# Kernel optimization log

Measured on AMD Instinct MI355X. Metric: run time of the kernel, lower is better.

Reference implementation:

```python
import jax, jax.numpy as jnp
import numpy as np
import math

H, Dh, S = 8, 64, 3          # heads, dim per head, samples factor
B, T, N, K = 2, 12, 512, 16  # batch, time, nodes, local-adj width
F = H * Dh                   # features = 512
SN = int(S * math.log2(N))   # Sampled_Nodes = 27
EPS = 1e-5


def setup_inputs() -> dict:
    key = jax.random.key(0)
    ks = jax.random.split(key, 22)
    sc = 1.0 / math.sqrt(F)
    W = lambda k: jax.random.normal(k, (F, F), jnp.float32) * sc
    bb = lambda k: jax.random.normal(k, (F,), jnp.float32) * 0.01
    return {
        "x": jax.random.normal(ks[0], (B, T, N, F), jnp.float32),
        "spa_eigvalue": jax.random.normal(ks[1], (F,), jnp.float32) * 0.1,
        "spa_eigvec": jax.random.normal(ks[2], (N, F), jnp.float32) * 0.1,
        "tem_eigvalue": jax.random.normal(ks[3], (F,), jnp.float32) * 0.1,
        "tem_eigvec": jax.random.normal(ks[4], (N, F), jnp.float32) * 0.1,
        "localadj": jax.random.randint(ks[5], (N, K), 0, N),
        "Wq": W(ks[6]), "bq": bb(ks[7]),
        "Wk": W(ks[8]), "bk": bb(ks[9]),
        "Wv": W(ks[10]), "bv": bb(ks[11]),
        "Wo": W(ks[12]), "bo": bb(ks[13]),
        "w_proj": jax.random.normal(ks[14], (K,), jnp.float32) / math.sqrt(K),
        "b_proj": jax.random.normal(ks[15], (), jnp.float32) * 0.01,
        "gamma": jnp.ones((F,), jnp.float32),
        "beta": jnp.zeros((F,), jnp.float32),
        "W1": W(ks[16]), "b1": bb(ks[17]),
        "W2": W(ks[18]), "b2": bb(ks[19]),
    }


def _lin(v, Wm, bv):  # torch nn.Linear: y = x @ W^T + b, W is [out, in]
    return jnp.einsum('...i,oi->...o', v, Wm) + bv


def _ln(v, g=None, b=None):  # LayerNorm over last dim, eps=1e-5
    mu = jnp.mean(v, -1, keepdims=True)
    var = jnp.var(v, -1, keepdims=True)
    y = (v - mu) * jax.lax.rsqrt(var + EPS)
    return y * g + b if g is not None else y


def reference(x, spa_eigvalue, spa_eigvec, tem_eigvalue, tem_eigvec, localadj,
              Wq, bq, Wk, bk, Wv, bv, Wo, bo, w_proj, b_proj,
              gamma, beta, W1, b1, W2, b2):
    # eigvec @ diag(eigval) == row-wise scaling
    x_ = x + (spa_eigvec * spa_eigvalue + tem_eigvec * tem_eigvalue)
    to_heads = lambda v: v.reshape(B, T, N, H, Dh).transpose(3, 0, 1, 2, 4)  # [H,B,T,N,Dh]
    Qh = to_heads(_lin(x_, Wq, bq))
    Kh = to_heads(_lin(x_, Wk, bk))
    Vh = to_heads(_lin(x_, Wv, bv))
    # local-adjacency K sampling: [H,B,T,N,K,Dh]
    Ks = Kh[:, :, :, localadj, :]
    qks = jnp.einsum('hbtnd,hbtnkd->hbtnk', Qh, Ks)
    # importance score per query node via learned projection over K neighbors
    M = jnp.einsum('hbtnk,k->hbtn', qks, w_proj) + b_proj
    _, m_top = jax.lax.top_k(M, SN)                              # [H,B,T,SN]
    Qr = jnp.take_along_axis(Qh, m_top[..., None], axis=3)       # [H,B,T,SN,Dh]
    scores = jnp.einsum('hbtsd,hbtnd->hbtsn', Qr, Kh) / math.sqrt(Dh)
    attn = jax.nn.softmax(scores, axis=-1)                       # [H,B,T,SN,N]
    cp = jnp.argmax(attn, axis=-2)                               # best sampled query per key node [H,B,T,N]
    val = jnp.einsum('hbtsn,hbtnd->hbtsd', attn, Vh)             # [H,B,T,SN,Dh]
    out = jnp.take_along_axis(val, cp[..., None], axis=3)        # [H,B,T,N,Dh]
    out = out.transpose(1, 2, 3, 0, 4).reshape(B, T, N, F)       # merge heads
    v = _ln(_lin(out, Wo, bo), gamma, beta)
    h = jax.nn.relu(_lin(v, W1, b1))
    h = _lin(h, W2, b2) + v
    return _ln(h)
```

## Files before the change

### kernel.cpp

```cpp
#include <hip/hip_runtime.h>
#include <math.h>

#define H_    8
#define DH    64
#define NN    512
#define KADJ  16
#define FF    512
#define BTOT  24
#define ROWS  12288
#define SN_   27
#define EPS_  1e-5f

typedef short short8 __attribute__((ext_vector_type(8)));
typedef float f32x4  __attribute__((ext_vector_type(4)));

__device__ __forceinline__ ushort f2bf(float x) {
    uint u = __float_as_uint(x);
    u += 0x7FFFu + ((u >> 16) & 1u);
    return (ushort)(u >> 16);
}
__device__ __forceinline__ float bf2f(ushort h) {
    return __uint_as_float(((uint)h) << 16);
}
__device__ __forceinline__ void pack_hilo(float4 a, float4 b, short8& hi, short8& lo) {
    float v[8] = {a.x, a.y, a.z, a.w, b.x, b.y, b.z, b.w};
    #pragma unroll
    for (int j = 0; j < 8; ++j) {
        ushort h = f2bf(v[j]);
        hi[j] = (short)h;
        lo[j] = (short)f2bf(v[j] - bf2f(h));
    }
}

__device__ __forceinline__ void gload_lds16(const ushort* g, ushort* l) {
    __builtin_amdgcn_global_load_lds(
        (const __attribute__((address_space(1))) unsigned int*)g,
        (__attribute__((address_space(3))) unsigned int*)l,
        16, 0, 0);
}

__global__ __launch_bounds__(256) void add_pos_bf16(
    const float* __restrict__ x,
    const float* __restrict__ spa_val, const float* __restrict__ spa_vec,
    const float* __restrict__ tem_val, const float* __restrict__ tem_vec,
    ushort* __restrict__ xh, ushort* __restrict__ xl)
{
    int i = blockIdx.x * 256 + threadIdx.x;
    int f4  = i & 127;
    int row = i >> 7;
    int n   = row & (NN - 1);

    float4 xv = reinterpret_cast<const float4*>(x)[i];
    float4 sv = reinterpret_cast<const float4*>(spa_vec)[n * 128 + f4];
    float4 tv = reinterpret_cast<const float4*>(tem_vec)[n * 128 + f4];
    float4 se = reinterpret_cast<const float4*>(spa_val)[f4];
    float4 te = reinterpret_cast<const float4*>(tem_val)[f4];
    float r0 = xv.x + sv.x * se.x + tv.x * te.x;
    float r1 = xv.y + sv.y * se.y + tv.y * te.y;
    float r2 = xv.z + sv.z * se.z + tv.z * te.z;
    float r3 = xv.w + sv.w * se.w + tv.w * te.w;
    ushort h0 = f2bf(r0), h1 = f2bf(r1), h2 = f2bf(r2), h3 = f2bf(r3);
    reinterpret_cast<ushort4*>(xh)[i] = make_ushort4(h0, h1, h2, h3);
    reinterpret_cast<ushort4*>(xl)[i] = make_ushort4(
        f2bf(r0 - bf2f(h0)), f2bf(r1 - bf2f(h1)),
        f2bf(r2 - bf2f(h2)), f2bf(r3 - bf2f(h3)));
}

__global__ __launch_bounds__(256) void wconv_kernel(
    const float* __restrict__ w0, const float* __restrict__ w1,
    const float* __restrict__ w2, const float* __restrict__ w3,
    const float* __restrict__ w4, const float* __restrict__ w5,
    ushort* __restrict__ whi, ushort* __restrict__ wlo)
{
    const int wi = blockIdx.y;
    const float* W = wi == 0 ? w0 : wi == 1 ? w1 : wi == 2 ? w2 :
                     wi == 3 ? w3 : wi == 4 ? w4 : w5;
    int i = blockIdx.x * 256 + threadIdx.x;
    float4 v = reinterpret_cast<const float4*>(W)[i];
    ushort h0 = f2bf(v.x), h1 = f2bf(v.y), h2 = f2bf(v.z), h3 = f2bf(v.w);
    reinterpret_cast<ushort4*>(whi + (size_t)wi * 262144)[i] =
        make_ushort4(h0, h1, h2, h3);
    if (wi < 2) {
        reinterpret_cast<ushort4*>(wlo + (size_t)wi * 262144)[i] =
            make_ushort4(f2bf(v.x - bf2f(h0)), f2bf(v.y - bf2f(h1)),
                         f2bf(v.z - bf2f(h2)), f2bf(v.w - bf2f(h3)));
    }
}

#define GBM 64
#define GBN 128

template <int SPLIT, int EPI, int OUTBF>
__global__ __launch_bounds__(256, 2) void gemm_mfma2(
    const ushort* __restrict__ Ah, const ushort* __restrict__ Al,
    const ushort* __restrict__ Wh, const ushort* __restrict__ Wl,
    const float* __restrict__ bias, const float* __restrict__ addsrc,
    float* __restrict__ Cf, ushort* __restrict__ Cb)
{
    __shared__ ushort sA[GBM * 64];
    __shared__ ushort sB[GBN * 64];

    const int nx  = gridDim.x >> 3;
    const int bid = blockIdx.x;
    const int lt  = (bid & 7) * nx + (bid >> 3);
    const int rowBase = (lt >> 2) * GBM;
    const int colBase = (lt & 3) * GBN;

    const int tid  = threadIdx.x;
    const int lane = tid & 63;
    const int wid  = tid >> 6;
    const int q    = lane >> 4;
    const int fr   = lane & 15;
    const int wm   = wid & 1;
    const int wn   = wid >> 1;

    const int kadv = SPLIT ? 32 : 64;
    const ushort* asrc[2];
    const ushort* bsrc[4];
    #pragma unroll
    for (int c = 0; c < 2; ++c) {
        const int p   = wid * 2048 + c * 1024 + lane * 16;
        const int row = p >> 7;
        const int ss  = ((p >> 4) & 7) ^ (row & 7);
        if (!SPLIT)
            asrc[c] = Ah + (size_t)(rowBase + row) * FF + ss * 8;
        else
            asrc[c] = (ss < 4)
                ? Ah + (size_t)(rowBase + row) * FF + ss * 8
                : Al + (size_t)(rowBase + row) * FF + (ss - 4) * 8;
    }
    #pragma unroll
    for (int c = 0; c < 4; ++c) {
        const int p   = wid * 4096 + c * 1024 + lane * 16;
        const int row = p >> 7;
        const int ss  = ((p >> 4) & 7) ^ (row & 7);
        if (!SPLIT)
            bsrc[c] = Wh + (size_t)(colBase + row) * FF + ss * 8;
        else
            bsrc[c] = (ss < 4)
                ? Wh + (size_t)(colBase + row) * FF + ss * 8
                : Wl + (size_t)(colBase + row) * FF + (ss - 4) * 8;
    }

    f32x4 acc[2][4];
    #pragma unroll
    for (int mi = 0; mi < 2; ++mi)
        #pragma unroll
        for (int ni = 0; ni < 4; ++ni) acc[mi][ni] = (f32x4){0.f, 0.f, 0.f, 0.f};

    const int NSTEP = SPLIT ? 16 : 8;
    const int swz = fr & 7;

    for (int step = 0; step < NSTEP; ++step) {
        #pragma unroll
        for (int c = 0; c < 2; ++c) {
            gload_lds16(asrc[c], &sA[wid * 1024 + c * 512]);
            asrc[c] += kadv;
        }
        #pragma unroll
        for (int c = 0; c < 4; ++c) {
            gload_lds16(bsrc[c], &sB[wid * 2048 + c * 512]);
            bsrc[c] += kadv;
        }
        __syncthreads();

        if (!SPLIT) {
            #pragma unroll
            for (int ksub = 0; ksub < 2; ++ksub) {
                const int kq = ksub * 4 + q;
                short8 af[2], bf[4];
                #pragma unroll
                for (int mi = 0; mi < 2; ++mi)
                    af[mi] = *(const short8*)&sA[(wm * 32 + mi * 16 + fr) * 64 +
                                                 ((kq ^ swz) << 3)];
                #pragma unroll
                for (int ni = 0; ni < 4; ++ni)
                    bf[ni] = *(const short8*)&sB[(wn * 64 + ni * 16 + fr) * 64 +
                                                 ((kq ^ swz) << 3)];
                #pragma unroll
                for (int mi = 0; mi < 2; ++mi)
                    #pragma unroll
                    for (int ni = 0; ni < 4; ++ni)
                        acc[mi][ni] = __builtin_amdgcn_mfma_f32_16x16x32_bf16(
                            af[mi], bf[ni], acc[mi][ni], 0, 0, 0);
            }
        } else {
            short8 ah[2], bh[4], t[4];
            #pragma unroll
            for (int mi = 0; mi < 2; ++mi)
                ah[mi] = *(const short8*)&sA[(wm * 32 + mi * 16 + fr) * 64 +
                                             ((q ^ swz) << 3)];
            #pragma unroll
            for (int ni = 0; ni < 4; ++ni)
                bh[ni] = *(const short8*)&sB[(wn * 64 + ni * 16 + fr) * 64 +
                                             ((q ^ swz) << 3)];
            #pragma unroll
            for (int mi = 0; mi < 2; ++mi)
                #pragma unroll
                for (int ni = 0; ni < 4; ++ni)
                    acc[mi][ni] = __builtin_amdgcn_mfma_f32_16x16x32_bf16(
                        ah[mi], bh[ni], acc[mi][ni], 0, 0, 0);
            #pragma unroll
            for (int ni = 0; ni < 4; ++ni)
                t[ni] = *(const short8*)&sB[(wn * 64 + ni * 16 + fr) * 64 +
                                            (((q + 4) ^ swz) << 3)];
            #pragma unroll
            for (int mi = 0; mi < 2; ++mi)
                #pragma unroll
                for (int ni = 0; ni < 4; ++ni)
                    acc[mi][ni] = __builtin_amdgcn_mfma_f32_16x16x32_bf16(
                        ah[mi], t[ni], acc[mi][ni], 0, 0, 0);
            #pragma unroll
            for (int mi = 0; mi < 2; ++mi)
                t[mi] = *(const short8*)&sA[(wm * 32 + mi * 16 + fr) * 64 +
                                            (((q + 4) ^ swz) << 3)];
            #pragma unroll
            for (int mi = 0; mi < 2; ++mi)
                #pragma unroll
                for (int ni = 0; ni < 4; ++ni)
                    acc[mi][ni] = __builtin_amdgcn_mfma_f32_16x16x32_bf16(
                        t[mi], bh[ni], acc[mi][ni], 0, 0, 0);
        }
        __syncthreads();
    }

    #pragma unroll
    for (int mi = 0; mi < 2; ++mi)
        #pragma unroll
        for (int ni = 0; ni < 4; ++ni) {
            const int col = colBase + wn * 64 + ni * 16 + fr;
            const float bcol = bias[col];
            #pragma unroll
            for (int r = 0; r < 4; ++r) {
                const int row = rowBase + wm * 32 + mi * 16 + q * 4 + r;
                float v = acc[mi][ni][r] + bcol;
                if (EPI == 1) v = fmaxf(v, 0.0f);
                if (EPI == 2) v += addsrc[(size_t)row * FF + col];
                if (OUTBF) Cb[(size_t)row * FF + col] = f2bf(v);
                else       Cf[(size_t)row * FF + col] = v;
            }
        }
}

__global__ __launch_bounds__(256) void qks_M_kernel(
    const float* __restrict__ Q, const float* __restrict__ K,
    const int* __restrict__ adj, const float* __restrict__ w_proj,
    const float* __restrict__ b_proj, float* __restrict__ Mout)
{
    const int w = blockIdx.x * 4 + (threadIdx.x >> 6);
    const int lane = threadIdx.x & 63;
    const int n   = w & (NN - 1);
    const int hbt = w >> 9;
    const int h   = hbt / BTOT;
    const int bt  = hbt % BTOT;

    float s = 0.0f;
    #pragma unroll
    for (int k = 0; k < KADJ; ++k) {
        const int j = adj[n * KADJ + k];
        s += w_proj[k] * K[((size_t)(bt * NN + j)) * FF + h * DH + lane];
    }
    float t = Q[((size_t)(bt * NN + n)) * FF + h * DH + lane] * s;
    #pragma unroll
    for (int o = 32; o; o >>= 1) t += __shfl_xor(t, o);
    if (lane == 0) Mout[(size_t)hbt * NN + n] = t + b_proj[0];
}

__global__ __launch_bounds__(64) void topk_kernel(
    const float* __restrict__ M, int* __restrict__ mtop)
{
    const int g = blockIdx.x;
    __shared__ float vals[NN];
    const int lane = threadIdx.x;
    for (int i = lane; i < NN; i += 64) vals[i] = M[(size_t)g * NN + i];
    __syncthreads();

    for (int s = 0; s < SN_; ++s) {
        float bv = -INFINITY;
        int bi = 1 << 30;
        for (int i = lane; i < NN; i += 64) {
            float v = vals[i];
            if (v > bv || (v == bv && i < bi)) { bv = v; bi = i; }
        }
        #pragma unroll
        for (int o = 32; o; o >>= 1) {
            float ov = __shfl_xor(bv, o);
            int   oi = __shfl_xor(bi, o);
            if (ov > bv || (ov == bv && oi < bi)) { bv = ov; bi = oi; }
        }
        if (lane == 0) {
            mtop[g * SN_ + s] = bi;
            vals[bi] = -INFINITY;
        }
        __syncthreads();
    }
}

__global__ __launch_bounds__(512) void fused_attn(
    const float* __restrict__ Q, const float* __restrict__ K,
    const float* __restrict__ V, const int* __restrict__ mtop,
    ushort* __restrict__ attnout)
{
    __shared__ ushort P_lds[32 * 512];
    __shared__ float red0[8][32];
    __shared__ float red1[8][32];
    __shared__ float val_lds[32][68];
    __shared__ int   cp_lds[NN];
    __shared__ int   mt[32];

    const int g = blockIdx.x;
    const int h = g / BTOT, bt = g % BTOT;
    const int tid = threadIdx.x;
    const int wave = tid >> 6, lane = tid & 63;
    const int q = lane >> 4, c = lane & 15;
    const size_t base_bt = (size_t)bt * NN * FF;
    const int hcol = h * DH;

    if (tid < 32) mt[tid] = mtop[g * SN_ + (tid < SN_ ? tid : 0)];
    __syncthreads();

    short8 afh[2][2], afl[2][2];
    #pragma unroll
    for (int m = 0; m < 2; ++m) {
        const int grow = mt[m * 16 + c];
        const float* qp = Q + base_bt + (size_t)grow * FF + hcol + q * 8;
        #pragma unroll
        for (int ks = 0; ks < 2; ++ks) {
            float4 a0 = *(const float4*)(qp + ks * 32);
            float4 a1 = *(const float4*)(qp + ks * 32 + 4);
            pack_hilo(a0, a1, afh[m][ks], afl[m][ks]);
        }
    }

    const int n0 = wave * 64;
    short8 bfh[4][2], bfl[4][2];
    #pragma unroll
    for (int nt = 0; nt < 4; ++nt) {
        const int krow = n0 + nt * 16 + c;
        const float* kp = K + base_bt + (size_t)krow * FF + hcol + q * 8;
        #pragma unroll
        for (int ks = 0; ks < 2; ++ks) {
            float4 b0 = *(const float4*)(kp + ks * 32);
            float4 b1 = *(const float4*)(kp + ks * 32 + 4);
            pack_hilo(b0, b1, bfh[nt][ks], bfl[nt][ks]);
        }
    }

    f32x4 sc[2][4];
    #pragma unroll
    for (int m = 0; m < 2; ++m)
        #pragma unroll
        for (int nt = 0; nt < 4; ++nt) sc[m][nt] = (f32x4){0.f, 0.f, 0.f, 0.f};
    #pragma unroll
    for (int ks = 0; ks < 2; ++ks)
        #pragma unroll
        for (int m = 0; m < 2; ++m)
            #pragma unroll
            for (int nt = 0; nt < 4; ++nt) {
                sc[m][nt] = __builtin_amdgcn_mfma_f32_16x16x32_bf16(
                    afh[m][ks], bfh[nt][ks], sc[m][nt], 0, 0, 0);
                sc[m][nt] = __builtin_amdgcn_mfma_f32_16x16x32_bf16(
                    afh[m][ks], bfl[nt][ks], sc[m][nt], 0, 0, 0);
                sc[m][nt] = __builtin_amdgcn_mfma_f32_16x16x32_bf16(
                    afl[m][ks], bfh[nt][ks], sc[m][nt], 0, 0, 0);
            }
    #pragma unroll
    for (int m = 0; m < 2; ++m)
        #pragma unroll
        for (int nt = 0; nt < 4; ++nt)
            #pragma unroll
            for (int r = 0; r < 4; ++r) sc[m][nt][r] *= 0.125f;

    float rmax[2][4];
    #pragma unroll
    for (int m = 0; m < 2; ++m)
        #pragma unroll
        for (int r = 0; r < 4; ++r) {
            float v = sc[m][0][r];
            v = fmaxf(v, sc[m][1][r]);
            v = fmaxf(v, sc[m][2][r]);
            v = fmaxf(v, sc[m][3][r]);
            rmax[m][r] = v;
        }
    #pragma unroll
    for (int off = 1; off <= 8; off <<= 1)
        #pragma unroll
        for (int m = 0; m < 2; ++m)
            #pragma unroll
            for (int r = 0; r < 4; ++r)
                rmax[m][r] = fmaxf(rmax[m][r], __shfl_xor(rmax[m][r], off));
    if (c == 0) {
        #pragma unroll
        for (int m = 0; m < 2; ++m)
            #pragma unroll
            for (int r = 0; r < 4; ++r)
                red0[wave][m * 16 + q * 4 + r] = rmax[m][r];
    }
    __syncthreads();
    float gmax[2][4];
    #pragma unroll
    for (int m = 0; m < 2; ++m)
        #pragma unroll
        for (int r = 0; r < 4; ++r) {
            const int row = m * 16 + q * 4 + r;
            float v = red0[0][row];
            #pragma unroll
            for (int w = 1; w < 8; ++w) v = fmaxf(v, red0[w][row]);
            gmax[m][r] = v;
        }

    float rsum[2][4] = {};
    #pragma unroll
    for (int m = 0; m < 2; ++m)
        #pragma unroll
        for (int nt = 0; nt < 4; ++nt)
            #pragma unroll
            for (int r = 0; r < 4; ++r) {
                float e = expf(sc[m][nt][r] - gmax[m][r]);
                sc[m][nt][r] = e;
                rsum[m][r] += e;
            }
    #pragma unroll
    for (int off = 1; off <= 8; off <<= 1)
        #pragma unroll
        for (int m = 0; m < 2; ++m)
            #pragma unroll
            for (int r = 0; r < 4; ++r)
                rsum[m][r] += __shfl_xor(rsum[m][r], off);
    if (c == 0) {
        #pragma unroll
        for (int m = 0; m < 2; ++m)
            #pragma unroll
            for (int r = 0; r < 4; ++r)
                red1[wave][m * 16 + q * 4 + r] = rsum[m][r];
    }
    __syncthreads();
    #pragma unroll
    for (int m = 0; m < 2; ++m)
        #pragma unroll
        for (int r = 0; r < 4; ++r) {
            const int row = m * 16 + q * 4 + r;
            float s = red1[0][row];
            #pragma unroll
            for (int w = 1; w < 8; ++w) s += red1[w][row];
            const float inv = 1.0f / s;
            #pragma unroll
            for (int nt = 0; nt < 4; ++nt) sc[m][nt][r] *= inv;
        }

    #pragma unroll
    for (int nt = 0; nt < 4; ++nt) {
        float bv = -INFINITY;
        int bi = 1 << 30;
        #pragma unroll
        for (int m = 0; m < 2; ++m)
            #pragma unroll
            for (int r = 0; r < 4; ++r) {
                const int row = m * 16 + q * 4 + r;
                if (row < SN_) {
                    float v = sc[m][nt][r];
                    if (v > bv) { bv = v; bi = row; }
                }
            }
        #pragma unroll
        for (int off = 16; off <= 32; off <<= 1) {
            float ov = __shfl_xor(bv, off);
            int   oi = __shfl_xor(bi, off);
            if (ov > bv || (ov == bv && oi < bi)) { bv = ov; bi = oi; }
        }
        if (q == 0) cp_lds[n0 + nt * 16 + c] = bi;
    }

    #pragma unroll
    for (int m = 0; m < 2; ++m)
        #pragma unroll
        for (int nt = 0; nt < 4; ++nt)
            #pragma unroll
            for (int r = 0; r < 4; ++r) {
                const int row = m * 16 + q * 4 + r;
                const int col = n0 + nt * 16 + c;
                P_lds[(row * 512 + col) ^ ((row & 7) << 3)] = f2bf(sc[m][nt][r]);
            }
    __syncthreads();

    const int msel = wave >> 2, dt = wave & 3;
    const int dcol = hcol + dt * 16 + c;
    const float* vb = V + base_bt + dcol;
    const int prow = msel * 16 + c;
    const int pswz = (prow & 7) << 3;
    f32x4 acc = (f32x4){0.f, 0.f, 0.f, 0.f};
    for (int kstep = 0; kstep < 16; ++kstep) {
        short8 a = *(const short8*)&P_lds[(prow * 512 + kstep * 32 + q * 8) ^ pswz];
        short8 b;
        #pragma unroll
        for (int j = 0; j < 8; ++j)
            b[j] = (short)f2bf(vb[(size_t)(kstep * 32 + q * 8 + j) * FF]);
        acc = __builtin_amdgcn_mfma_f32_16x16x32_bf16(a, b, acc, 0, 0, 0);
    }
    #pragma unroll
    for (int r = 0; r < 4; ++r)
        val_lds[msel * 16 + q * 4 + r][dt * 16 + c] = acc[r];
    __syncthreads();

    #pragma unroll
    for (int pass = 0; pass < 8; ++pass) {
        const int n  = pass * 64 + (tid >> 3);
        const int s  = cp_lds[n];
        const int d0 = (tid & 7) * 8;
        const float* vr = &val_lds[s][d0];
        uint4 u;
        u.x = (uint)f2bf(vr[0]) | ((uint)f2bf(vr[1]) << 16);
        u.y = (uint)f2bf(vr[2]) | ((uint)f2bf(vr[3]) << 16);
        u.z = (uint)f2bf(vr[4]) | ((uint)f2bf(vr[5]) << 16);
        u.w = (uint)f2bf(vr[6]) | ((uint)f2bf(vr[7]) << 16);
        *(uint4*)(attnout + base_bt + (size_t)n * FF + hcol + d0) = u;
    }
}

template <int AFFINE, int BFOUT>
__global__ __launch_bounds__(256) void ln_kernel(
    const float* __restrict__ X, const float* __restrict__ g,
    const float* __restrict__ b, float* __restrict__ Yf,
    ushort* __restrict__ Yb, int rows)
{
    const int row = blockIdx.x * 4 + (threadIdx.x >> 6);
    if (row >= rows) return;
    const int lane = threadIdx.x & 63;
    const float4* x4 = reinterpret_cast<const float4*>(X + (size_t)row * FF);
    float4 a = x4[lane];
    float4 c = x4[lane + 64];
    float s = a.x + a.y + a.z + a.w + c.x + c.y + c.z + c.w;
    float q = a.x * a.x + a.y * a.y + a.z * a.z + a.w * a.w +
              c.x * c.x + c.y * c.y + c.z * c.z + c.w * c.w;
    #pragma unroll
    for (int o = 32; o; o >>= 1) {
        s += __shfl_xor(s, o);
        q += __shfl_xor(q, o);
    }
    const float mu   = s * (1.0f / FF);
    const float var  = q * (1.0f / FF) - mu * mu;
    const float rstd = 1.0f / sqrtf(var + EPS_);

    float4 ya, yc;
    ya.x = (a.x - mu) * rstd; ya.y = (a.y - mu) * rstd;
    ya.z = (a.z - mu) * rstd; ya.w = (a.w - mu) * rstd;
    yc.x = (c.x - mu) * rstd; yc.y = (c.y - mu) * rstd;
    yc.z = (c.z - mu) * rstd; yc.w = (c.w - mu) * rstd;
    if (AFFINE) {
        float4 ga = reinterpret_cast<const float4*>(g)[lane];
        float4 gc = reinterpret_cast<const float4*>(g)[lane + 64];
        float4 ba = reinterpret_cast<const float4*>(b)[lane];
        float4 bc = reinterpret_cast<const float4*>(b)[lane + 64];
        ya.x = ya.x * ga.x + ba.x; ya.y = ya.y * ga.y + ba.y;
        ya.z = ya.z * ga.z + ba.z; ya.w = ya.w * ga.w + ba.w;
        yc.x = yc.x * gc.x + bc.x; yc.y = yc.y * gc.y + bc.y;
        yc.z = yc.z * gc.z + bc.z; yc.w = yc.w * gc.w + bc.w;
    }
    float4* y4 = reinterpret_cast<float4*>(Yf + (size_t)row * FF);
    y4[lane]      = ya;
    y4[lane + 64] = yc;
    if (BFOUT) {
        ushort4* yb = reinterpret_cast<ushort4*>(Yb + (size_t)row * FF);
        yb[lane] = make_ushort4(f2bf(ya.x), f2bf(ya.y), f2bf(ya.z), f2bf(ya.w));
        yb[lane + 64] = make_ushort4(f2bf(yc.x), f2bf(yc.y), f2bf(yc.z), f2bf(yc.w));
    }
}

extern "C" void kernel_launch(void* const* d_in, const int* in_sizes, int n_in,
                              void* d_out, int out_size, void* d_ws, size_t ws_size,
                              hipStream_t stream)
{
    const float* x       = (const float*)d_in[0];
    const float* spa_val = (const float*)d_in[1];
    const float* spa_vec = (const float*)d_in[2];
    const float* tem_val = (const float*)d_in[3];
    const float* tem_vec = (const float*)d_in[4];
    const int*   adj     = (const int*)  d_in[5];
    const float* Wq = (const float*)d_in[6];  const float* bq = (const float*)d_in[7];
    const float* Wk = (const float*)d_in[8];  const float* bk = (const float*)d_in[9];
    const float* Wv = (const float*)d_in[10]; const float* bv = (const float*)d_in[11];
    const float* Wo = (const float*)d_in[12]; const float* bo = (const float*)d_in[13];
    const float* w_proj = (const float*)d_in[14];
    const float* b_proj = (const float*)d_in[15];
    const float* gamma  = (const float*)d_in[16];
    const float* beta   = (const float*)d_in[17];
    const float* W1 = (const float*)d_in[18]; const float* b1 = (const float*)d_in[19];
    const float* W2 = (const float*)d_in[20]; const float* b2 = (const float*)d_in[21];

    float* out = (float*)d_out;
    float* ws  = (float*)d_ws;

    const size_t R = (size_t)ROWS * FF;

    float* bufQ = ws;
    float* bufK = ws + R;
    float* bufV = ws + 2 * R;
    ushort* whi = (ushort*)(ws + 3 * R);
    ushort* wlo = whi + 6 * 262144;
    float* Mbuf = ws + 3 * R + (6 * 262144 + 2 * 262144) / 2;
    int*   mtop = (int*)(Mbuf + (size_t)H_ * BTOT * NN);

    ushort* xh  = (ushort*)d_out;
    ushort* xl  = xh + R;
    ushort* attnout = xh;
    ushort* vbf = xl;
    ushort* h1b = xh;

    add_pos_bf16<<<(ROWS * FF / 4) / 256, 256, 0, stream>>>(
        x, spa_val, spa_vec, tem_val, tem_vec, xh, xl);

    wconv_kernel<<<dim3(256, 6), 256, 0, stream>>>(Wq, Wk, Wv, Wo, W1, W2, whi, wlo);

    const int NG = (ROWS / GBM) * (FF / GBN);
    gemm_mfma2<1, 0, 0><<<NG, 256, 0, stream>>>(xh, xl, whi, wlo, bq, nullptr, bufQ, nullptr);
    gemm_mfma2<1, 0, 0><<<NG, 256, 0, stream>>>(xh, xl, whi + 262144, wlo + 262144, bk, nullptr, bufK, nullptr);
    gemm_mfma2<0, 0, 0><<<NG, 256, 0, stream>>>(xh, nullptr, whi + 2 * 262144, nullptr, bv, nullptr, bufV, nullptr);

    qks_M_kernel<<<(H_ * BTOT * NN) / 4, 256, 0, stream>>>(
        bufQ, bufK, adj, w_proj, b_proj, Mbuf);
    topk_kernel<<<H_ * BTOT, 64, 0, stream>>>(Mbuf, mtop);

    fused_attn<<<H_ * BTOT, 512, 0, stream>>>(bufQ, bufK, bufV, mtop, attnout);

    gemm_mfma2<0, 0, 0><<<NG, 256, 0, stream>>>(attnout, nullptr, whi + 3 * 262144, nullptr, bo, nullptr, bufQ, nullptr);
    ln_kernel<1, 1><<<ROWS / 4, 256, 0, stream>>>(bufQ, gamma, beta, bufK, vbf, ROWS);
    gemm_mfma2<0, 1, 1><<<NG, 256, 0, stream>>>(vbf, nullptr, whi + 4 * 262144, nullptr, b1, nullptr, nullptr, h1b);
    gemm_mfma2<0, 2, 0><<<NG, 256, 0, stream>>>(h1b, nullptr, whi + 5 * 262144, nullptr, b2, bufK, bufV, nullptr);
    ln_kernel<0, 0><<<ROWS / 4, 256, 0, stream>>>(bufV, nullptr, nullptr, out, nullptr, ROWS);
}
```

Before: 236.6 us.

## Prefetch V tile into registers and stage transposed bf16 V in LDS

The V slice for each head is now loaded with coalesced float4 loads at kernel start, which hides its latency behind the QK and softmax phases. It is then converted to bf16 and written transposed into a swizzled LDS buffer. The PV MFMA loop reads B fragments from LDS as short8 vectors instead of doing strided scalar global loads with per-element conversion. The cost is 64 KB of extra LDS and 64 more live registers per thread, which may reduce occupancy or cause spills.

```diff
diff --git a/kernel.cpp b/kernel.cpp
--- a/kernel.cpp
+++ b/kernel.cpp
@@ -302,6 +302,7 @@
     ushort* __restrict__ attnout)
 {
     __shared__ ushort P_lds[32 * 512];
+    __shared__ ushort Vt_lds[64 * 512];
     __shared__ float red0[8][32];
     __shared__ float red1[8][32];
     __shared__ float val_lds[32][68];
@@ -317,6 +318,17 @@
     const int hcol = h * DH;
 
     if (tid < 32) mt[tid] = mtop[g * SN_ + (tid < SN_ ? tid : 0)];
+
+    float4 vreg[4][4];
+    #pragma unroll
+    for (int i = 0; i < 4; ++i) {
+        const int u  = tid + i * 512;
+        const int d4 = u & 15, ng = u >> 4;
+        const float* vp = V + base_bt + (size_t)(ng * 4) * FF + hcol + d4 * 4;
+        #pragma unroll
+        for (int ii = 0; ii < 4; ++ii)
+            vreg[i][ii] = *(const float4*)(vp + (size_t)ii * FF);
+    }
     __syncthreads();
 
     short8 afh[2][2], afl[2][2];
@@ -481,20 +493,35 @@
                 const int col = n0 + nt * 16 + c;
                 P_lds[(row * 512 + col) ^ ((row & 7) << 3)] = f2bf(sc[m][nt][r]);
             }
+
+    #pragma unroll
+    for (int i = 0; i < 4; ++i) {
+        const int u  = tid + i * 512;
+        const int d4 = u & 15, ng = u >> 4;
+        const int n0v = ng * 4;
+        #pragma unroll
+        for (int j = 0; j < 4; ++j) {
+            const int d = d4 * 4 + j;
+            ushort4 t;
+            t.x = f2bf(((const float*)&vreg[i][0])[j]);
+            t.y = f2bf(((const float*)&vreg[i][1])[j]);
+            t.z = f2bf(((const float*)&vreg[i][2])[j]);
+            t.w = f2bf(((const float*)&vreg[i][3])[j]);
+            const int addr = (d * 512 + n0v) ^ ((d & 7) << 3);
+            *(ushort4*)&Vt_lds[addr] = t;
+        }
+    }
     __syncthreads();
 
     const int msel = wave >> 2, dt = wave & 3;
-    const int dcol = hcol + dt * 16 + c;
-    const float* vb = V + base_bt + dcol;
+    const int dcol = dt * 16 + c;
     const int prow = msel * 16 + c;
     const int pswz = (prow & 7) << 3;
+    const int vswz = (dcol & 7) << 3;
     f32x4 acc = (f32x4){0.f, 0.f, 0.f, 0.f};
     for (int kstep = 0; kstep < 16; ++kstep) {
         short8 a = *(const short8*)&P_lds[(prow * 512 + kstep * 32 + q * 8) ^ pswz];
-        short8 b;
-        #pragma unroll
-        for (int j = 0; j < 8; ++j)
-            b[j] = (short)f2bf(vb[(size_t)(kstep * 32 + q * 8 + j) * FF]);
+        short8 b = *(const short8*)&Vt_lds[(dcol * 512 + kstep * 32 + q * 8) ^ vswz];
         acc = __builtin_amdgcn_mfma_f32_16x16x32_bf16(a, b, acc, 0, 0, 0);
     }
     #pragma unroll
```

New measurement: 234.9 us. No clear change (-0.7%).
